# Performance work log

Hardware: AMD Instinct MI355X
Metric: run time of the kernel (lower is better)

The kernel has to match this reference:

```python
import jax, jax.numpy as jnp
import numpy as np

B, D1, D = 8192, 512, 256
N_NEG = 100
ALPHA = 0.9          # mixup positivity
TAU_AUG = 1e-6       # L_aug temperature
TAU_SUPP = 1e-10     # L_supp temperature
EPS = 1e-6
REG_W, AUG_W, SUPP_W = 1e-4, 0.1, 1e-3


def setup_inputs() -> dict:
    key = jax.random.key(0)
    ks = jax.random.split(key, 9)
    return {
        "e1": jax.random.normal(ks[0], (B, D1), jnp.float32),
        "e2": jax.random.normal(ks[1], (B, D), jnp.float32),
        "y_pred": jax.random.normal(ks[2], (B, 1), jnp.float32),
        "y_target": jax.random.normal(ks[3], (B, 1), jnp.float32),
        "W_e2": jax.random.normal(ks[4], (D1, D), jnp.float32) / np.sqrt(D1),
        "lmbda_u": jax.random.uniform(ks[5], (B,), jnp.float32),
        "domain_tag": jax.random.randint(ks[6], (B,), 0, 4),
        "aug_neg_idx": jax.random.randint(ks[7], (B,), 0, B - 1),
        "neg_idx": jax.random.randint(ks[8], (B, N_NEG), 0, B - 1),
    }


def reference(e1, e2, y_pred, y_target, W_e2, lmbda_u, domain_tag, aug_neg_idx, neg_idx):
    # --- mse + L2 regularization (model params = W_e2 of e2_model) ---
    mse = jnp.mean(jnp.abs(y_pred - y_target))
    reg = REG_W * jnp.linalg.norm(W_e2)

    j = jnp.arange(B)
    # --- create_aug: mixup with a random negative (indices exclude self via shift) ---
    lmbda = ALPHA + (1.0 - ALPHA) * lmbda_u                       # [B] in [alpha, 1)
    a_idx = aug_neg_idx + (aug_neg_idx >= j)                      # != j
    aug_e1 = lmbda[:, None] * e1 + (1.0 - lmbda)[:, None] * e1[a_idx]
    phi_aug = aug_e1 @ W_e2                                       # e2_model(aug_e1): [B, D]

    # --- L_aug: InfoNCE-style ratio, batched over all rows ---
    pos = jnp.exp(TAU_AUG * jnp.sum(phi_aug * e2, axis=1))        # [B]
    n_idx = neg_idx + (neg_idx >= j[:, None])                     # [B, N_NEG], != j
    neg = jnp.exp(TAU_AUG * jnp.einsum('bnd,bd->bn', phi_aug[n_idx], e2))
    L_aug_rows = jnp.log(pos / (EPS + pos + jnp.sum(neg, axis=1)))
    aug_loss = AUG_W * (-jnp.mean(L_aug_rows))

    # --- L_supp: domain-contrastive on full B x B similarity ---
    S = jnp.exp(TAU_SUPP * (e2 @ e2.T))                           # [B, B]
    diff = (domain_tag[None, :] != domain_tag[:, None]).astype(S.dtype)
    nom = jnp.sum(S * diff, axis=1)                               # different-domain mass
    den = jnp.sum(S, axis=1)                                      # all-samples mass
    valid = jnp.sum(diff, axis=1) > 0                             # skip rows with no other domain
    L_supp_rows = jnp.where(valid, jnp.log(jnp.where(valid, nom, 1.0) / (den + EPS)), 0.0)
    supp_loss = SUPP_W * (-jnp.sum(L_supp_rows) / B)

    return mse + reg + aug_loss + supp_loss
```

## Files before the change

### kernel.cpp

```cpp
#include <hip/hip_runtime.h>
#include <stdint.h>

#define B_    8192
#define D1_   512
#define D_    256
#define NNEG  100

typedef __attribute__((ext_vector_type(8))) short bf16x8;
typedef __attribute__((ext_vector_type(4))) short bf16x4;
typedef __attribute__((ext_vector_type(4))) float f32x4;

static __device__ __forceinline__ short f2bf(float f) {
  union { float f; unsigned u; } c; c.f = f;
  unsigned r = (c.u + 0x7FFFu + ((c.u >> 16) & 1u)) >> 16;
  return (short)r;
}
static __device__ __forceinline__ float bf2f(short s) {
  union { unsigned u; float f; } c; c.u = ((unsigned)(unsigned short)s) << 16;
  return c.f;
}

__global__ void k0_init(float* wsf, int* hist) {
  if (threadIdx.x < 4) wsf[threadIdx.x] = 0.f;
  if (threadIdx.x >= 4 && threadIdx.x < 8) hist[threadIdx.x - 4] = 0;
}

__global__ __launch_bounds__(256) void kA_pre(const float* __restrict__ W,
                                              short* __restrict__ Wt,
                                              const float* __restrict__ yp,
                                              const float* __restrict__ yt,
                                              const int* __restrict__ tag,
                                              float* wsf, int* hist) {
  const int t = blockIdx.x * 256 + threadIdx.x;
  const int lane = threadIdx.x & 63, wv = threadIdx.x >> 6;
  __shared__ float lw[4], lm[4];
  __shared__ int lh[4];
  if (threadIdx.x < 4) lh[threadIdx.x] = 0;
  __syncthreads();

  const int k = t >> 8, n = t & 255;
  float w = W[t];
  Wt[n * 512 + k] = f2bf(w);
  float s = w * w;

  float d = 0.f;
  if (t < 8192) {
    d = fabsf(yp[t] - yt[t]);
    atomicAdd(&lh[tag[t]], 1);
  }
  #pragma unroll
  for (int off = 32; off; off >>= 1) {
    s += __shfl_down(s, off);
    d += __shfl_down(d, off);
  }
  if (lane == 0) { lw[wv] = s; lm[wv] = d; }
  __syncthreads();
  if (threadIdx.x == 0) {
    atomicAdd(&wsf[1], lw[0] + lw[1] + lw[2] + lw[3]);
    float dm = lm[0] + lm[1] + lm[2] + lm[3];
    if (dm != 0.f || blockIdx.x < 32) atomicAdd(&wsf[0], dm);
  }
  if (threadIdx.x < 4 && lh[threadIdx.x] != 0)
    atomicAdd(&hist[threadIdx.x], lh[threadIdx.x]);
}

__global__ __launch_bounds__(1024) void k3_gemm(const float* __restrict__ e1,
                                                const float* __restrict__ lu,
                                                const int* __restrict__ aidx,
                                                const short* __restrict__ Wt,
                                                short* __restrict__ phi) {
  __shared__ short As[16 * 512];
  char* asb = (char*)As;
  const int t = threadIdx.x;
  const int bm0 = blockIdx.x * 16;

  {
    const int r = t >> 6;
    const int row = bm0 + r;
    const float lmv = 0.9f + 0.1f * lu[row];
    const float omv = 1.f - lmv;
    int an = aidx[row];
    int a2 = an + (an >= row);
    const float* px = e1 + (long)row * D1_;
    const float* py = e1 + (long)a2 * D1_;
    const int c0 = (t & 63) * 4;
    #pragma unroll
    for (int j = 0; j < 2; ++j) {
      const int c = c0 + j * 256;
      float4 x = *(const float4*)(px + c);
      float4 y = *(const float4*)(py + c);
      bf16x4 o;
      o[0] = f2bf(lmv * x.x + omv * y.x);
      o[1] = f2bf(lmv * x.y + omv * y.y);
      o[2] = f2bf(lmv * x.z + omv * y.z);
      o[3] = f2bf(lmv * x.w + omv * y.w);
      *(bf16x4*)(asb + r * 1024 + ((c * 2) ^ ((r & 7) << 4))) = o;
    }
  }
  __syncthreads();

  const int lane = t & 63, wv = t >> 6;
  const int lo = lane & 15, hi = lane >> 4;
  const short* wb = Wt + (wv * 16 + lo) * 512;

  f32x4 acc = {};
  #pragma unroll
  for (int kk = 0; kk < 16; ++kk) {
    bf16x8 a = *(const bf16x8*)(asb + lo * 1024 + ((kk * 64 + hi * 16) ^ ((lo & 7) << 4)));
    bf16x8 b = *(const bf16x8*)(wb + kk * 32 + hi * 8);
    acc = __builtin_amdgcn_mfma_f32_16x16x32_bf16(a, b, acc, 0, 0, 0);
  }
  #pragma unroll
  for (int q = 0; q < 4; ++q) {
    int R = bm0 + hi * 4 + q;
    phi[R * D_ + wv * 16 + lo] = f2bf(acc[q]);
  }
}

__global__ __launch_bounds__(256) void k4_neg(const short* __restrict__ phi,
                                              const float* __restrict__ e2,
                                              const int* __restrict__ nidx,
                                              float* wsf) {
  const int lane = threadIdx.x & 63;
  const int wv   = threadIdx.x >> 6;
  const int b    = blockIdx.x * 4 + wv;
  const int h    = lane >> 5;
  const int q    = lane & 31;

  const int* nrow = nidx + b * NNEG;
  float acc[8] = {0.f, 0.f, 0.f, 0.f, 0.f, 0.f, 0.f, 0.f};

  #pragma unroll 1
  for (int it = 0; it < 10; ++it) {
    bf16x8 v[5];
    #pragma unroll
    for (int u = 0; u < 5; ++u) {
      int i = (it * 5 + u) * 2 + h;
      int nn = nrow[i];
      int r = nn + (nn >= b);
      v[u] = *(const bf16x8*)(phi + (long)r * D_ + q * 8);
    }
    #pragma unroll
    for (int u = 0; u < 5; ++u)
      #pragma unroll
      for (int j = 0; j < 8; ++j)
        acc[j] += bf2f(v[u][j]);
  }

  const float* er = e2 + (long)b * D_ + q * 8;
  float ev[8];
  *(float4*)&ev[0] = *(const float4*)(er);
  *(float4*)&ev[4] = *(const float4*)(er + 4);
  bf16x8 pb = *(const bf16x8*)(phi + (long)b * D_ + q * 8);

  float sneg = 0.f, spos = 0.f;
  #pragma unroll
  for (int j = 0; j < 8; ++j) {
    sneg += acc[j] * ev[j];
    spos += bf2f(pb[j]) * ev[j];
  }
  #pragma unroll
  for (int off = 1; off <= 32; off <<= 1) {
    sneg += __shfl_xor(sneg, off);
    spos += __shfl_xor(spos, off);
  }

  __shared__ float lrow[4];
  if (lane == 0) {
    spos *= 0.5f;
    float pos  = 1.f + 1e-6f * spos;
    float negs = 100.f + 1e-6f * sneg;
    lrow[wv] = logf(pos / (1e-6f + pos + negs));
  }
  __syncthreads();
  if (threadIdx.x == 0)
    atomicAdd(&wsf[2], lrow[0] + lrow[1] + lrow[2] + lrow[3]);
}

__global__ void k5_fin(const float* wsf, const int* hist, float* out) {
  if (threadIdx.x == 0 && blockIdx.x == 0) {
    float mse = wsf[0] * (1.f / 8192.f);
    float reg = 1e-4f * sqrtf(wsf[1]);
    float aug = 0.1f * (-wsf[2] * (1.f / 8192.f));
    float ss = 0.f;
    for (int t = 0; t < 4; ++t) {
      int c = hist[t];
      int cd = B_ - c;
      if (c > 0 && cd > 0)
        ss += (float)c * logf((float)cd / (8192.f + 1e-6f));
    }
    float supp = 1e-3f * (-ss * (1.f / 8192.f));
    out[0] = mse + reg + aug + supp;
  }
}

extern "C" void kernel_launch(void* const* d_in, const int* in_sizes, int n_in,
                              void* d_out, int out_size, void* d_ws, size_t ws_size,
                              hipStream_t stream) {
  const float* e1  = (const float*)d_in[0];
  const float* e2  = (const float*)d_in[1];
  const float* yp  = (const float*)d_in[2];
  const float* yt  = (const float*)d_in[3];
  const float* W   = (const float*)d_in[4];
  const float* lu  = (const float*)d_in[5];
  const int*   tag = (const int*)d_in[6];
  const int*   aix = (const int*)d_in[7];
  const int*   nix = (const int*)d_in[8];
  float* out = (float*)d_out;

  char* ws    = (char*)d_ws;
  float* wsf  = (float*)ws;
  int*   hist = (int*)(ws + 16);
  short* Wt   = (short*)(ws + 256);
  short* phi  = (short*)(ws + 256 + 262144);

  k0_init<<<1, 64, 0, stream>>>(wsf, hist);
  kA_pre<<<512, 256, 0, stream>>>(W, Wt, yp, yt, tag, wsf, hist);
  k3_gemm<<<512, 1024, 0, stream>>>(e1, lu, aix, Wt, phi);
  k4_neg<<<2048, 256, 0, stream>>>(phi, e2, nix, wsf);
  k5_fin<<<1, 64, 0, stream>>>(wsf, hist, out);
}
```

Baseline: 152.7 us.

## Fuse finalize into neg kernel via last-block ticket and stage neg indices in LDS

Drops the separate init and finalize kernels. The workspace is now zeroed with a memset, and the last block of the negative-gather kernel computes the final scalar after taking an atomic ticket. Negative indices are loaded cooperatively into shared memory with the self-skip shift applied up front, and row indices for the next iteration are prefetched so that gather addresses no longer wait on global index loads. This removes two launches and some index-load latency, at the cost of an extra fence and atomic per block.

Result: slower. 189.6 us (+24.2%).

```diff
diff --git a/kernel.cpp b/kernel.cpp
--- a/kernel.cpp
+++ b/kernel.cpp
@@ -20,10 +20,6 @@
   return c.f;
 }
 
-__global__ void k0_init(float* wsf, int* hist) {
-  if (threadIdx.x < 4) wsf[threadIdx.x] = 0.f;
-  if (threadIdx.x >= 4 && threadIdx.x < 8) hist[threadIdx.x - 4] = 0;
-}
 
 __global__ __launch_bounds__(256) void kA_pre(const float* __restrict__ W,
                                               short* __restrict__ Wt,
@@ -120,25 +116,42 @@
 __global__ __launch_bounds__(256) void k4_neg(const short* __restrict__ phi,
                                               const float* __restrict__ e2,
                                               const int* __restrict__ nidx,
-                                              float* wsf) {
+                                              float* wsf, int* hist,
+                                              int* ticket, float* out) {
+  __shared__ int sidx[4 * NNEG];
+  __shared__ float lrow[4];
+  __shared__ int isLast;
+
+  #pragma unroll
+  for (int e = threadIdx.x; e < 4 * NNEG; e += 256) {
+    int nn = nidx[blockIdx.x * 4 * NNEG + e];
+    int bb = blockIdx.x * 4 + e / NNEG;
+    sidx[e] = nn + (nn >= bb);
+  }
+  __syncthreads();
+
   const int lane = threadIdx.x & 63;
   const int wv   = threadIdx.x >> 6;
   const int b    = blockIdx.x * 4 + wv;
   const int h    = lane >> 5;
   const int q    = lane & 31;
 
-  const int* nrow = nidx + b * NNEG;
+  const int base = wv * NNEG + h * 50;
   float acc[8] = {0.f, 0.f, 0.f, 0.f, 0.f, 0.f, 0.f, 0.f};
+
+  int rn[5];
+  #pragma unroll
+  for (int u = 0; u < 5; ++u) rn[u] = sidx[base + u];
 
   #pragma unroll 1
   for (int it = 0; it < 10; ++it) {
     bf16x8 v[5];
     #pragma unroll
-    for (int u = 0; u < 5; ++u) {
-      int i = (it * 5 + u) * 2 + h;
-      int nn = nrow[i];
-      int r = nn + (nn >= b);
-      v[u] = *(const bf16x8*)(phi + (long)r * D_ + q * 8);
+    for (int u = 0; u < 5; ++u)
+      v[u] = *(const bf16x8*)(phi + (long)rn[u] * D_ + q * 8);
+    if (it < 9) {
+      #pragma unroll
+      for (int u = 0; u < 5; ++u) rn[u] = sidx[base + (it + 1) * 5 + u];
     }
     #pragma unroll
     for (int u = 0; u < 5; ++u)
@@ -165,7 +178,6 @@
     spos += __shfl_xor(spos, off);
   }
 
-  __shared__ float lrow[4];
   if (lane == 0) {
     spos *= 0.5f;
     float pos  = 1.f + 1e-6f * spos;
@@ -173,15 +185,21 @@
     lrow[wv] = logf(pos / (1e-6f + pos + negs));
   }
   __syncthreads();
-  if (threadIdx.x == 0)
+
+  if (threadIdx.x == 0) {
     atomicAdd(&wsf[2], lrow[0] + lrow[1] + lrow[2] + lrow[3]);
-}
-
-__global__ void k5_fin(const float* wsf, const int* hist, float* out) {
-  if (threadIdx.x == 0 && blockIdx.x == 0) {
+    __threadfence();
+    int tk = atomicAdd(ticket, 1);
+    isLast = (tk == (int)gridDim.x - 1);
+  }
+  __syncthreads();
+
+  if (isLast && threadIdx.x == 0) {
+    __threadfence();
+    float augsum = atomicAdd(&wsf[2], 0.f);
     float mse = wsf[0] * (1.f / 8192.f);
     float reg = 1e-4f * sqrtf(wsf[1]);
-    float aug = 0.1f * (-wsf[2] * (1.f / 8192.f));
+    float aug = 0.1f * (-augsum * (1.f / 8192.f));
     float ss = 0.f;
     for (int t = 0; t < 4; ++t) {
       int c = hist[t];
@@ -208,15 +226,15 @@
   const int*   nix = (const int*)d_in[8];
   float* out = (float*)d_out;
 
-  char* ws    = (char*)d_ws;
-  float* wsf  = (float*)ws;
-  int*   hist = (int*)(ws + 16);
-  short* Wt   = (short*)(ws + 256);
-  short* phi  = (short*)(ws + 256 + 262144);
-
-  k0_init<<<1, 64, 0, stream>>>(wsf, hist);
+  char* ws     = (char*)d_ws;
+  float* wsf   = (float*)ws;
+  int*   hist  = (int*)(ws + 32);
+  int*   ticket= (int*)(ws + 48);
+  short* Wt    = (short*)(ws + 256);
+  short* phi   = (short*)(ws + 256 + 262144);
+
+  hipMemsetAsync(ws, 0, 64, stream);
   kA_pre<<<512, 256, 0, stream>>>(W, Wt, yp, yt, tag, wsf, hist);
   k3_gemm<<<512, 1024, 0, stream>>>(e1, lu, aix, Wt, phi);
-  k4_neg<<<2048, 256, 0, stream>>>(phi, e2, nix, wsf);
-  k5_fin<<<1, 64, 0, stream>>>(wsf, hist, out);
-}
+  k4_neg<<<2048, 256, 0, stream>>>(phi, e2, nix, wsf, hist, ticket, out);
+}
```
